# Kernel optimization log

Measured on AMD Instinct MI355X. Metric: run time of the kernel, lower is better.

## Reference

```python
import jax, jax.numpy as jnp
import numpy as np

BN_EPS = 1e-5

def _l2norm(x):
    n = jnp.sqrt(jnp.sum(x * x, axis=-1, keepdims=True))
    return x / jnp.maximum(n, 1e-12)

def _bn_eval(x, gamma, beta):
    # eval-mode BatchNorm2d (running_mean=0, running_var=1)
    g = gamma / jnp.sqrt(1.0 + BN_EPS)
    return x * g[None, :, None, None] + beta[None, :, None, None]

def _forward(feat, Wq, Wk, Wv, ad_conv_w, ad_conv_b, pm_w1, pm_w2,
             back_w, catt, catt1, mlp_w, mlp_b, mlp_gamma, mlp_beta,
             dsn_w, dsn_b, dsn_gamma, dsn_beta):
    B, C, H, W = feat.shape
    p = pm_w1.shape[1]  # p_num (top-k size)
    x2d = feat.reshape(B, C, H * W).transpose(0, 2, 1)          # [B,HW,C]
    q = jnp.einsum('bnc,dc->bnd', x2d, Wq)                       # [B,HW,cim]
    k = jnp.einsum('bnc,dc->bnd', x2d, Wk)
    v = jnp.einsum('bnc,dc->bnd', x2d, Wv)
    # cosine-similarity attention weights [B,HW,HW]
    w = jnp.einsum('bid,bjd->bij', _l2norm(q), _l2norm(k))
    wv, idx = jax.lax.top_k(w, p)                                # [B,HW,p]
    vg = jax.vmap(lambda vv, ii: vv[ii])(v, idx)                 # [B,HW,p,cim] gather
    # ADConv: 1x1 conv on a single channel == scalar affine
    xa = wv * ad_conv_w[0] + ad_conv_b[0]
    pos = jnp.where(xa > 0, xa, 0.0)
    hdn = jax.nn.relu(jnp.einsum('bip,qp->biq', pos, pm_w1))     # [B,HW,2p]
    mask = jax.nn.sigmoid(jnp.einsum('biq,pq->bip', hdn, pm_w2)) # [B,HW,p]
    att = jax.nn.softmax(jnp.where(xa > 0, xa, -100000.0), axis=-1)
    wfin = att * mask                                            # [B,HW,p]
    ov = jnp.einsum('bip,bipd->bid', wfin, vg)                   # [B,HW,cim]
    ov = jnp.einsum('bid,cd->bic', ov, back_w)                   # [B,HW,C]
    v_img = catt * ov.transpose(0, 2, 1).reshape(B, C, H, W)
    cat = jnp.concatenate([v_img, catt1 * feat], axis=1)         # [B,2C,H,W]
    x = jnp.einsum('oc,bchw->bohw', mlp_w, cat) + mlp_b[None, :, None, None]
    x = jax.nn.relu(_bn_eval(x, mlp_gamma, mlp_beta))
    r0 = jnp.einsum('oc,bchw->bohw', dsn_w, x) + dsn_b[None, :, None, None]
    r0 = jax.nn.relu(_bn_eval(r0, dsn_gamma, dsn_beta))
    return x, r0

def setup_inputs() -> dict:
    key = jax.random.key(0)
    ks = jax.random.split(key, 12)
    B, C, H, W = 2, 256, 80, 80
    cim, p = C // 8, 9
    sc = 0.05
    return {
        'feat': jax.random.normal(ks[0], (B, C, H, W), jnp.float32),
        'Wq': jax.random.normal(ks[1], (cim, C), jnp.float32) * sc,
        'Wk': jax.random.normal(ks[2], (cim, C), jnp.float32) * sc,
        'Wv': jax.random.normal(ks[3], (cim, C), jnp.float32) * sc,
        'ad_conv_w': jnp.ones((1,), jnp.float32),
        'ad_conv_b': jnp.zeros((1,), jnp.float32),
        'pm_w1': jax.random.normal(ks[4], (2 * p, p), jnp.float32) * 0.3,
        'pm_w2': jax.random.normal(ks[5], (p, 2 * p), jnp.float32) * 0.3,
        'back_w': jax.random.normal(ks[6], (C, cim), jnp.float32) * sc,
        'catt': jnp.ones((1, C, 1, 1), jnp.float32),
        'catt1': jnp.ones((1, C, 1, 1), jnp.float32),
        'mlp_w': jax.random.normal(ks[7], (C, 2 * C), jnp.float32) * sc,
        'mlp_b': jnp.zeros((C,), jnp.float32),
        'mlp_gamma': jnp.ones((C,), jnp.float32),
        'mlp_beta': jnp.zeros((C,), jnp.float32),
        'dsn_w': jax.random.normal(ks[8], (1, C), jnp.float32) * sc,
        'dsn_b': jnp.zeros((1,), jnp.float32),
        'dsn_gamma': jnp.ones((1,), jnp.float32),
        'dsn_beta': jnp.zeros((1,), jnp.float32),
        'H': H,
        'W': W,
    }

def reference(feat, Wq, Wk, Wv, ad_conv_w, ad_conv_b, pm_w1, pm_w2,
              back_w, catt, catt1, mlp_w, mlp_b, mlp_gamma, mlp_beta,
              dsn_w, dsn_b, dsn_gamma, dsn_beta, H, W):
    # H,W < 768 -> get_forward branch
    return _forward(feat, Wq, Wk, Wv, ad_conv_w, ad_conv_b, pm_w1, pm_w2,
                    back_w, catt, catt1, mlp_w, mlp_b, mlp_gamma, mlp_beta,
                    dsn_w, dsn_b, dsn_gamma, dsn_beta)
```

## Files before the change

### kernel.cpp

```cpp
#include <hip/hip_runtime.h>
#include <hip/hip_bf16.h>

#define HW   6400
#define NB   2
#define CC   256
#define CIM  32
#define PP   9
#define P2   18
#define ROWS (NB*HW)
#define NCH  16
#define JCH  (HW/NCH)
#define NGRP (ROWS/64)

#define OFF_QN   0
#define OFF_KN   (OFF_QN + ROWS*CIM)
#define OFF_V    (OFF_KN + ROWS*CIM)
#define OFF_OV   (OFF_V  + ROWS*CIM)
#define OFF_PV   (OFF_OV + ROWS*CIM)
#define OFF_PI   (OFF_PV + ROWS*NCH*PP)
#define OFF_W1T  (OFF_PI + ROWS*NCH*PP)
#define OFF_W2T  (OFF_W1T + CIM*CC)
#define OFF_BF   (OFF_W2T + CC*CC)
#define OFF_WQT  (OFF_BF + CC)
#define OFF_WKT  (OFF_WQT + CC*CIM)
#define OFF_WVT  (OFF_WKT + CC*CIM)

__global__ void prep_kernel(const float* __restrict__ mlp_w, const float* __restrict__ mlp_b,
                            const float* __restrict__ mlp_g, const float* __restrict__ mlp_be,
                            const float* __restrict__ back_w, const float* __restrict__ catt,
                            const float* __restrict__ catt1,
                            const float* __restrict__ Wq, const float* __restrict__ Wk,
                            const float* __restrict__ Wv, float* __restrict__ ws) {
    const int blk = blockIdx.x, t = threadIdx.x;
    const float bnc = rsqrtf(1.0f + 1e-5f);
    if (blk < 32) {
        const int d = blk, o = t;
        const float g = mlp_g[o] * bnc;
        float acc = 0.f;
        for (int c = 0; c < CC; ++c)
            acc = fmaf(mlp_w[o*512 + c] * catt[c], back_w[c*CIM + d], acc);
        ws[OFF_W1T + d*CC + o] = g * acc;
    } else if (blk == 32) {
        const int o = t;
        const float g = mlp_g[o] * bnc;
        for (int c = 0; c < CC; ++c)
            ws[OFF_W2T + c*CC + o] = g * mlp_w[o*512 + 256 + c] * catt1[c];
        ws[OFF_BF + o] = g * mlp_b[o] + mlp_be[o];
    } else {
        const float* W = (blk == 33) ? Wq : (blk == 34) ? Wk : Wv;
        float* WT = ws + ((blk == 33) ? OFF_WQT : (blk == 34) ? OFF_WKT : OFF_WVT);
        for (int i = t; i < CC*CIM; i += 256) {
            const int c = i / CIM, d = i % CIM;
            WT[c*CIM + d] = W[d*CC + c];
        }
    }
}

__global__ __launch_bounds__(256) void qkv_kernel(const float* __restrict__ feat,
                                                  const float* __restrict__ ws_r,
                                                  float* __restrict__ ws) {
    __shared__ float part[4][64][33];
    __shared__ float invA[64];
    const int bx = blockIdx.x;
    const int mat = bx % 3;
    const int ng  = bx / 3;
    const int n0  = ng * 64;
    const int b   = n0 / HW;
    const int nsp0 = n0 % HW;
    const int tid = threadIdx.x;
    const int w = __builtin_amdgcn_readfirstlane(tid >> 6);
    const int lane = tid & 63;
    const float* WT = ws_r + (mat == 0 ? OFF_WQT : mat == 1 ? OFF_WKT : OFF_WVT);
    const float* fbase = feat + (size_t)b*CC*HW + nsp0 + lane;
    float acc[CIM];
#pragma unroll
    for (int d = 0; d < CIM; ++d) acc[d] = 0.f;
    const int c0 = w * 64;
    for (int cc = 0; cc < 64; ++cc) {
        const int c = c0 + cc;
        const float fv = fbase[(size_t)c * HW];
        const float* wt = WT + c*CIM;
#pragma unroll
        for (int d = 0; d < CIM; ++d) acc[d] = fmaf(fv, wt[d], acc[d]);
    }
#pragma unroll
    for (int d = 0; d < CIM; ++d) part[w][lane][d] = acc[d];
    __syncthreads();
    {
        const int n = tid >> 2, d0 = (tid & 3) * 8;
#pragma unroll
        for (int dd = 0; dd < 8; ++dd) {
            const int d = d0 + dd;
            part[0][n][d] = part[0][n][d] + part[1][n][d] + part[2][n][d] + part[3][n][d];
        }
    }
    __syncthreads();
    if (mat < 2) {
        if (tid < 64) {
            const int n = tid;
            float ss = 0.f;
#pragma unroll
            for (int d = 0; d < CIM; ++d) { const float x = part[0][n][d]; ss = fmaf(x, x, ss); }
            invA[n] = 1.0f / fmaxf(sqrtf(ss), 1e-12f);
        }
        __syncthreads();
    }
    float* outp = ws + (mat == 0 ? OFF_QN : mat == 1 ? OFF_KN : OFF_V);
    {
        const int n = tid >> 2, d0 = (tid & 3) * 8;
        const float scl = (mat < 2) ? invA[n] : 1.0f;
        const size_t r = (size_t)(n0 + n);
#pragma unroll
        for (int dd = 0; dd < 8; ++dd)
            outp[r*CIM + d0 + dd] = part[0][n][d0 + dd] * scl;
    }
}

__global__ __launch_bounds__(64) void attn_kernel(const float* __restrict__ ws_r,
                                                  float* __restrict__ ws) {
    const int bx = blockIdx.x;
    const int rg = bx >> 4;
    const int ch = bx & 15;
    const int lane = threadIdx.x;
    const int r = rg*64 + lane;
    const int b = (rg*64) / HW;
    const float* qn = ws_r + OFF_QN + (size_t)r*CIM;
    float q[CIM];
#pragma unroll
    for (int d = 0; d < CIM; ++d) q[d] = qn[d];
    const float* kbase = ws_r + OFF_KN + ((size_t)b*HW + ch*JCH)*CIM;
    float tv[PP]; int ti[PP];
#pragma unroll
    for (int s = 0; s < PP; ++s) { tv[s] = -3.0e38f; ti[s] = 0; }
#pragma unroll 2
    for (int j = 0; j < JCH; ++j) {
        const float* kp = kbase + j*CIM;
        float a0 = 0.f, a1 = 0.f, a2 = 0.f, a3 = 0.f;
#pragma unroll
        for (int d = 0; d < CIM; d += 4) {
            a0 = fmaf(q[d+0], kp[d+0], a0);
            a1 = fmaf(q[d+1], kp[d+1], a1);
            a2 = fmaf(q[d+2], kp[d+2], a2);
            a3 = fmaf(q[d+3], kp[d+3], a3);
        }
        const float wv = (a0 + a1) + (a2 + a3);
        if (wv > tv[8]) {
            tv[8] = wv; ti[8] = ch*JCH + j;
#pragma unroll
            for (int s = 8; s > 0; --s) {
                const bool sw = tv[s] > tv[s-1];
                const float vA = tv[s-1], vB = tv[s];
                tv[s-1] = sw ? vB : vA;  tv[s] = sw ? vA : vB;
                const int iA = ti[s-1], iB = ti[s];
                ti[s-1] = sw ? iB : iA;  ti[s] = sw ? iA : iB;
            }
        }
    }
    float* pv = ws + OFF_PV + ((size_t)r*NCH + ch)*PP;
    int*   pi = (int*)(ws + OFF_PI) + ((size_t)r*NCH + ch)*PP;
#pragma unroll
    for (int s = 0; s < PP; ++s) { pv[s] = tv[s]; pi[s] = ti[s]; }
}

__global__ __launch_bounds__(256) void merge_kernel(const float* __restrict__ ws_r,
                                                    const float* __restrict__ pm_w1,
                                                    const float* __restrict__ pm_w2,
                                                    const float* __restrict__ ad_w,
                                                    const float* __restrict__ ad_b,
                                                    float* __restrict__ ws) {
    __shared__ float pm1[P2*PP];
    __shared__ float pm2[PP*P2];
    const int tid = threadIdx.x;
    for (int i = tid; i < P2*PP; i += 256) pm1[i] = pm_w1[i];
    for (int i = tid; i < PP*P2; i += 256) pm2[i] = pm_w2[i];
    __syncthreads();
    const int w = tid >> 6, lane = tid & 63;
    const int r = blockIdx.x*4 + w;
    const int b = r / HW;
    const float* pv = ws_r + OFF_PV + (size_t)r*NCH*PP;
    const int*   pi = (const int*)(ws_r + OFF_PI) + (size_t)r*NCH*PP;
    float c0v = -3e38f, c1v = -3e38f, c2v = -3e38f;
    int   c0i = 0x7fffffff, c1i = 0x7fffffff, c2i = 0x7fffffff;
    { const int s = lane;       if (s < NCH*PP) { c0v = pv[s]; c0i = pi[s]; } }
    { const int s = lane + 64;  if (s < NCH*PP) { c1v = pv[s]; c1i = pi[s]; } }
    { const int s = lane + 128; if (s < NCH*PP) { c2v = pv[s]; c2i = pi[s]; } }
    float topv[PP]; int topi[PP];
#pragma unroll
    for (int rd = 0; rd < PP; ++rd) {
        float hv = c0v; int hi = c0i; int hw_ = 0;
        if (c1v > hv || (c1v == hv && c1i < hi)) { hv = c1v; hi = c1i; hw_ = 1; }
        if (c2v > hv || (c2v == hv && c2i < hi)) { hv = c2v; hi = c2i; hw_ = 2; }
        float bv = hv; int bi = hi;
#pragma unroll
        for (int off = 32; off >= 1; off >>= 1) {
            const float ov_ = __shfl_xor(bv, off);
            const int   oi_ = __shfl_xor(bi, off);
            if (ov_ > bv || (ov_ == bv && oi_ < bi)) { bv = ov_; bi = oi_; }
        }
        if (hv == bv && hi == bi) {
            if (hw_ == 0) c0v = -3e38f;
            else if (hw_ == 1) c1v = -3e38f;
            else c2v = -3e38f;
        }
        topv[rd] = bv;
        topi[rd] = (bi >= 0 && bi < HW) ? bi : 0;
    }
    const float adw = ad_w[0], adb = ad_b[0];
    float xa[PP], pos[PP];
#pragma unroll
    for (int p = 0; p < PP; ++p) { xa[p] = fmaf(topv[p], adw, adb); pos[p] = fmaxf(xa[p], 0.f); }
    float hdn[P2];
#pragma unroll
    for (int qq = 0; qq < P2; ++qq) {
        float a = 0.f;
#pragma unroll
        for (int p = 0; p < PP; ++p) a = fmaf(pos[p], pm1[qq*PP + p], a);
        hdn[qq] = fmaxf(a, 0.f);
    }
    float msk[PP];
#pragma unroll
    for (int p = 0; p < PP; ++p) {
        float a = 0.f;
#pragma unroll
        for (int qq = 0; qq < P2; ++qq) a = fmaf(hdn[qq], pm2[p*P2 + qq], a);
        msk[p] = 1.0f / (1.0f + expf(-a));
    }
    float xm[PP], m = -3e38f;
#pragma unroll
    for (int p = 0; p < PP; ++p) { xm[p] = xa[p] > 0.f ? xa[p] : -100000.0f; m = fmaxf(m, xm[p]); }
    float e[PP], ssum = 0.f;
#pragma unroll
    for (int p = 0; p < PP; ++p) { e[p] = expf(xm[p] - m); ssum += e[p]; }
    float wf[PP];
#pragma unroll
    for (int p = 0; p < PP; ++p) wf[p] = (e[p] / ssum) * msk[p];
    const int d = lane & 31;
    const float* vb = ws_r + OFF_V + (size_t)b*HW*CIM;
    float acc = 0.f;
#pragma unroll
    for (int p = 0; p < PP; ++p) acc = fmaf(wf[p], vb[(size_t)topi[p]*CIM + d], acc);
    if (lane < 32) ws[OFF_OV + (size_t)r*CIM + d] = acc;
}

__global__ __launch_bounds__(64) void fin_kernel(const float* __restrict__ feat,
                                                 const float* __restrict__ ws_r,
                                                 float* __restrict__ out) {
    __shared__ float ovt[64*33];
    const int bx = blockIdx.x;
    const int ng = bx % NGRP;
    const int og = bx / NGRP;
    const int n0 = ng*64;
    const int b  = n0 / HW;
    const int nsp0 = n0 % HW;
    const int lane = threadIdx.x;
    const float4* ovg = (const float4*)(ws_r + OFF_OV + (size_t)n0*CIM);
#pragma unroll
    for (int i = 0; i < 8; ++i) {
        const int f = lane + 64*i;
        const float4 vv = ovg[f];
        const int row = f >> 3, col = (f & 7) * 4;
        ovt[row*33 + col]     = vv.x;
        ovt[row*33 + col + 1] = vv.y;
        ovt[row*33 + col + 2] = vv.z;
        ovt[row*33 + col + 3] = vv.w;
    }
    __syncthreads();
    const int o0 = og * 16;
    float acc[16];
    const float* bfp = ws_r + OFF_BF;
#pragma unroll
    for (int oi = 0; oi < 16; ++oi) acc[oi] = bfp[o0 + oi];
    const float* w1t = ws_r + OFF_W1T;
#pragma unroll 4
    for (int dd = 0; dd < CIM; ++dd) {
        const float xv = ovt[lane*33 + dd];
        const float* wrow = w1t + dd*CC + o0;
#pragma unroll
        for (int oi = 0; oi < 16; ++oi) acc[oi] = fmaf(xv, wrow[oi], acc[oi]);
    }
    const float* w2t = ws_r + OFF_W2T;
    const float* fbase = feat + (size_t)b*CC*HW + nsp0 + lane;
#pragma unroll 4
    for (int c = 0; c < CC; ++c) {
        const float fv = fbase[(size_t)c * HW];
        const float* wrow = w2t + c*CC + o0;
#pragma unroll
        for (int oi = 0; oi < 16; ++oi) acc[oi] = fmaf(fv, wrow[oi], acc[oi]);
    }
    const size_t obase = (size_t)b*CC*HW + nsp0 + lane;
#pragma unroll
    for (int oi = 0; oi < 16; ++oi)
        out[obase + (size_t)(o0 + oi)*HW] = fmaxf(acc[oi], 0.f);
}

__global__ __launch_bounds__(256) void dsn_kernel(const float* __restrict__ xout,
                                                  const float* __restrict__ dsn_w,
                                                  const float* __restrict__ dsn_b,
                                                  const float* __restrict__ dsn_g,
                                                  const float* __restrict__ dsn_be,
                                                  float* __restrict__ out) {
    const int t = blockIdx.x*256 + threadIdx.x;
    const int b = t / HW, nsp = t % HW;
    const float* xb = xout + (size_t)b*CC*HW + nsp;
    float acc = 0.f;
#pragma unroll 4
    for (int o = 0; o < CC; ++o)
        acc = fmaf(xb[(size_t)o*HW], dsn_w[o], acc);
    const float g = dsn_g[0] * rsqrtf(1.0f + 1e-5f);
    const float r0 = fmaxf(fmaf(g, acc + dsn_b[0], dsn_be[0]), 0.f);
    out[(size_t)NB*CC*HW + t] = r0;
}

extern "C" void kernel_launch(void* const* d_in, const int* in_sizes, int n_in,
                              void* d_out, int out_size, void* d_ws, size_t ws_size,
                              hipStream_t stream) {
    const float* feat  = (const float*)d_in[0];
    const float* Wq    = (const float*)d_in[1];
    const float* Wk    = (const float*)d_in[2];
    const float* Wv    = (const float*)d_in[3];
    const float* adw   = (const float*)d_in[4];
    const float* adb   = (const float*)d_in[5];
    const float* pm_w1 = (const float*)d_in[6];
    const float* pm_w2 = (const float*)d_in[7];
    const float* backw = (const float*)d_in[8];
    const float* catt  = (const float*)d_in[9];
    const float* catt1 = (const float*)d_in[10];
    const float* mlp_w = (const float*)d_in[11];
    const float* mlp_b = (const float*)d_in[12];
    const float* mlp_g = (const float*)d_in[13];
    const float* mlp_be= (const float*)d_in[14];
    const float* dsn_w = (const float*)d_in[15];
    const float* dsn_b = (const float*)d_in[16];
    const float* dsn_g = (const float*)d_in[17];
    const float* dsn_be= (const float*)d_in[18];
    float* ws = (float*)d_ws;
    float* out = (float*)d_out;

    prep_kernel<<<36, 256, 0, stream>>>(mlp_w, mlp_b, mlp_g, mlp_be, backw, catt, catt1,
                                        Wq, Wk, Wv, ws);
    qkv_kernel<<<NGRP*3, 256, 0, stream>>>(feat, ws, ws);
    attn_kernel<<<NGRP*NCH, 64, 0, stream>>>(ws, ws);
    merge_kernel<<<ROWS/4, 256, 0, stream>>>(ws, pm_w1, pm_w2, adw, adb, ws);
    fin_kernel<<<NGRP*16, 64, 0, stream>>>(feat, ws, out);
    dsn_kernel<<<ROWS/256, 256, 0, stream>>>(out, dsn_w, dsn_b, dsn_g, dsn_be, out);
}
```

Before: 370.4 us.

## Double chunk split, packed-float dot, and register double-buffer K loads in attention

Splits each query's key range into 32 chunks instead of 16, so twice as many wavefronts scan shorter key ranges. Block size goes from 64 to 256 threads, with four wavefronts per block. The dot product uses 2-wide float vectors with elementwise FMA, and the next key row is loaded into registers while the current one is processed. The merge kernel is generalised to 5 candidate slots per lane to absorb the larger 288-entry partial top-k list, which adds merge and partial-buffer traffic in exchange for more parallelism in the dominant brute-force similarity scan.

Result: slower. 455.7 us (+23.0%).

```diff
diff --git a/kernel.cpp b/kernel.cpp
--- a/kernel.cpp
+++ b/kernel.cpp
@@ -8,9 +8,11 @@
 #define PP   9
 #define P2   18
 #define ROWS (NB*HW)
-#define NCH  16
+#define NCH  32
 #define JCH  (HW/NCH)
 #define NGRP (ROWS/64)
+
+typedef float f2 __attribute__((ext_vector_type(2)));
 
 #define OFF_QN   0
 #define OFF_KN   (OFF_QN + ROWS*CIM)
@@ -116,45 +118,61 @@
     }
 }
 
-__global__ __launch_bounds__(64) void attn_kernel(const float* __restrict__ ws_r,
-                                                  float* __restrict__ ws) {
-    const int bx = blockIdx.x;
-    const int rg = bx >> 4;
-    const int ch = bx & 15;
-    const int lane = threadIdx.x;
+#define LOADK(dst, jj)                                        \
+    {   const f2* kp_ = (const f2*)(kbase + (jj)*CIM);        \
+        _Pragma("unroll")                                     \
+        for (int h_ = 0; h_ < 16; ++h_) dst[h_] = kp_[h_];    }
+
+#define DOT_INSERT(kreg, jj)                                                  \
+    {   f2 a0 = {0.f,0.f}, a1 = {0.f,0.f}, a2 = {0.f,0.f}, a3 = {0.f,0.f};    \
+        _Pragma("unroll")                                                     \
+        for (int h_ = 0; h_ < 16; h_ += 4) {                                  \
+            a0 = __builtin_elementwise_fma(q[h_+0], kreg[h_+0], a0);          \
+            a1 = __builtin_elementwise_fma(q[h_+1], kreg[h_+1], a1);          \
+            a2 = __builtin_elementwise_fma(q[h_+2], kreg[h_+2], a2);          \
+            a3 = __builtin_elementwise_fma(q[h_+3], kreg[h_+3], a3);          \
+        }                                                                     \
+        f2 s0_ = a0 + a1, s1_ = a2 + a3;                                      \
+        f2 s_ = s0_ + s1_;                                                    \
+        const float wv_ = s_.x + s_.y;                                        \
+        if (wv_ > tv[8]) {                                                    \
+            tv[8] = wv_; ti[8] = jbase + (jj);                                \
+            _Pragma("unroll")                                                 \
+            for (int s = 8; s > 0; --s) {                                     \
+                const bool sw = tv[s] > tv[s-1];                              \
+                const float vA = tv[s-1], vB = tv[s];                         \
+                tv[s-1] = sw ? vB : vA;  tv[s] = sw ? vA : vB;                \
+                const int iA = ti[s-1], iB = ti[s];                           \
+                ti[s-1] = sw ? iB : iA;  ti[s] = sw ? iA : iB;                \
+            }                                                                 \
+        }                                                                     }
+
+__global__ __launch_bounds__(256) void attn_kernel(const float* __restrict__ ws_r,
+                                                   float* __restrict__ ws) {
+    const int tid  = threadIdx.x;
+    const int wid  = (blockIdx.x << 2) + (tid >> 6);
+    const int lane = tid & 63;
+    const int rg = wid >> 5;
+    const int ch = wid & (NCH-1);
     const int r = rg*64 + lane;
     const int b = (rg*64) / HW;
     const float* qn = ws_r + OFF_QN + (size_t)r*CIM;
-    float q[CIM];
-#pragma unroll
-    for (int d = 0; d < CIM; ++d) q[d] = qn[d];
+    f2 q[16];
+#pragma unroll
+    for (int h = 0; h < 16; ++h) q[h] = ((const f2*)qn)[h];
     const float* kbase = ws_r + OFF_KN + ((size_t)b*HW + ch*JCH)*CIM;
+    const int jbase = ch*JCH;
     float tv[PP]; int ti[PP];
 #pragma unroll
     for (int s = 0; s < PP; ++s) { tv[s] = -3.0e38f; ti[s] = 0; }
-#pragma unroll 2
-    for (int j = 0; j < JCH; ++j) {
-        const float* kp = kbase + j*CIM;
-        float a0 = 0.f, a1 = 0.f, a2 = 0.f, a3 = 0.f;
-#pragma unroll
-        for (int d = 0; d < CIM; d += 4) {
-            a0 = fmaf(q[d+0], kp[d+0], a0);
-            a1 = fmaf(q[d+1], kp[d+1], a1);
-            a2 = fmaf(q[d+2], kp[d+2], a2);
-            a3 = fmaf(q[d+3], kp[d+3], a3);
-        }
-        const float wv = (a0 + a1) + (a2 + a3);
-        if (wv > tv[8]) {
-            tv[8] = wv; ti[8] = ch*JCH + j;
-#pragma unroll
-            for (int s = 8; s > 0; --s) {
-                const bool sw = tv[s] > tv[s-1];
-                const float vA = tv[s-1], vB = tv[s];
-                tv[s-1] = sw ? vB : vA;  tv[s] = sw ? vA : vB;
-                const int iA = ti[s-1], iB = ti[s];
-                ti[s-1] = sw ? iB : iA;  ti[s] = sw ? iA : iB;
-            }
-        }
+    f2 ka[16], kb[16];
+    LOADK(ka, 0)
+    for (int j = 0; j < JCH; j += 2) {
+        LOADK(kb, j+1)
+        DOT_INSERT(ka, j)
+        const int j2 = (j+2 < JCH) ? (j+2) : (JCH-1);
+        LOADK(ka, j2)
+        DOT_INSERT(kb, j+1)
     }
     float* pv = ws + OFF_PV + ((size_t)r*NCH + ch)*PP;
     int*   pi = (int*)(ws + OFF_PI) + ((size_t)r*NCH + ch)*PP;
@@ -162,6 +180,7 @@
     for (int s = 0; s < PP; ++s) { pv[s] = tv[s]; pi[s] = ti[s]; }
 }
 
+#define NSLOT 5
 __global__ __launch_bounds__(256) void merge_kernel(const float* __restrict__ ws_r,
                                                     const float* __restrict__ pm_w1,
                                                     const float* __restrict__ pm_w2,
@@ -179,17 +198,20 @@
     const int b = r / HW;
     const float* pv = ws_r + OFF_PV + (size_t)r*NCH*PP;
     const int*   pi = (const int*)(ws_r + OFF_PI) + (size_t)r*NCH*PP;
-    float c0v = -3e38f, c1v = -3e38f, c2v = -3e38f;
-    int   c0i = 0x7fffffff, c1i = 0x7fffffff, c2i = 0x7fffffff;
-    { const int s = lane;       if (s < NCH*PP) { c0v = pv[s]; c0i = pi[s]; } }
-    { const int s = lane + 64;  if (s < NCH*PP) { c1v = pv[s]; c1i = pi[s]; } }
-    { const int s = lane + 128; if (s < NCH*PP) { c2v = pv[s]; c2i = pi[s]; } }
+    float cv[NSLOT]; int ci[NSLOT];
+#pragma unroll
+    for (int i = 0; i < NSLOT; ++i) {
+        const int s = lane + 64*i;
+        if (s < NCH*PP) { cv[i] = pv[s]; ci[i] = pi[s]; }
+        else            { cv[i] = -3e38f; ci[i] = 0x7fffffff; }
+    }
     float topv[PP]; int topi[PP];
 #pragma unroll
     for (int rd = 0; rd < PP; ++rd) {
-        float hv = c0v; int hi = c0i; int hw_ = 0;
-        if (c1v > hv || (c1v == hv && c1i < hi)) { hv = c1v; hi = c1i; hw_ = 1; }
-        if (c2v > hv || (c2v == hv && c2i < hi)) { hv = c2v; hi = c2i; hw_ = 2; }
+        float hv = cv[0]; int hi = ci[0]; int hs = 0;
+#pragma unroll
+        for (int i = 1; i < NSLOT; ++i)
+            if (cv[i] > hv || (cv[i] == hv && ci[i] < hi)) { hv = cv[i]; hi = ci[i]; hs = i; }
         float bv = hv; int bi = hi;
 #pragma unroll
         for (int off = 32; off >= 1; off >>= 1) {
@@ -197,11 +219,10 @@
             const int   oi_ = __shfl_xor(bi, off);
             if (ov_ > bv || (ov_ == bv && oi_ < bi)) { bv = ov_; bi = oi_; }
         }
-        if (hv == bv && hi == bi) {
-            if (hw_ == 0) c0v = -3e38f;
-            else if (hw_ == 1) c1v = -3e38f;
-            else c2v = -3e38f;
-        }
+        const bool won = (hv == bv && hi == bi);
+#pragma unroll
+        for (int i = 0; i < NSLOT; ++i)
+            if (won && i == hs) cv[i] = -3e38f;
         topv[rd] = bv;
         topi[rd] = (bi >= 0 && bi < HW) ? bi : 0;
     }
@@ -339,7 +360,7 @@
     prep_kernel<<<36, 256, 0, stream>>>(mlp_w, mlp_b, mlp_g, mlp_be, backw, catt, catt1,
                                         Wq, Wk, Wv, ws);
     qkv_kernel<<<NGRP*3, 256, 0, stream>>>(feat, ws, ws);
-    attn_kernel<<<NGRP*NCH, 64, 0, stream>>>(ws, ws);
+    attn_kernel<<<(NGRP*NCH)/4, 256, 0, stream>>>(ws, ws);
     merge_kernel<<<ROWS/4, 256, 0, stream>>>(ws, pm_w1, pm_w2, adw, adb, ws);
     fin_kernel<<<NGRP*16, 64, 0, stream>>>(feat, ws, out);
     dsn_kernel<<<ROWS/256, 256, 0, stream>>>(out, dsn_w, dsn_b, dsn_g, dsn_be, out);
```
